# Performance work log

Measured on AMD Instinct MI355X. Metric: run time of the kernel, lower is better.

## Reference

```python
import jax, jax.numpy as jnp
import numpy as np

NUM_SCALES = 4
ENC = 64
KMAX = 16
DT = 0.005  # base_time_constant; original code's (undefined) self.dt interpreted as this


def setup_inputs() -> dict:
    key = jax.random.key(0)
    ks = jax.random.split(key, 5)
    events = jax.random.normal(ks[0], (2, 2, 32, 32, 64), dtype=jnp.float32)
    # matches torch.logspace(-3, -1, num_scales)
    time_constants = jnp.logspace(-3.0, -1.0, NUM_SCALES).astype(jnp.float32)
    temporal_kernels = jax.random.normal(ks[1], (NUM_SCALES, ENC, KMAX), dtype=jnp.float32)
    w1 = jax.random.normal(ks[2], (2 * NUM_SCALES, NUM_SCALES), dtype=jnp.float32) * 0.1
    b1 = jnp.zeros((2 * NUM_SCALES,), dtype=jnp.float32)
    w2 = jax.random.normal(ks[3], (NUM_SCALES, 2 * NUM_SCALES), dtype=jnp.float32) * 0.1
    b2 = jnp.zeros((NUM_SCALES,), dtype=jnp.float32)
    return {"events": events, "time_constants": time_constants,
            "temporal_kernels": temporal_kernels, "w1": w1, "b1": b1, "w2": w2, "b2": b2}


def reference(events, time_constants, temporal_kernels, w1, b1, w2, b2):
    B, C, H, W, T = events.shape
    k = min(KMAX, T)
    # decay kernels per scale: [S, k], normalized to sum 1
    t_idx = jnp.arange(k, dtype=jnp.float32)
    decay = jnp.exp(-t_idx[None, :] * DT / time_constants[:, None])
    decay = decay / decay.sum(axis=-1, keepdims=True)
    # combined learnable kernels: [S, E, k]
    combined = decay[:, None, :] * temporal_kernels[:, :, :k]

    Cf = C * H * W
    # one batched cross-correlation (torch F.conv1d semantics == lax conv, no flip)
    x = events.reshape(B * Cf, 1, T)                       # [B*Cf, 1, T]
    kern = combined.reshape(NUM_SCALES * ENC, 1, k)        # [S*E, 1, k]
    out = jax.lax.conv_general_dilated(
        x, kern, window_strides=(1,), padding=[(k // 2, k // 2)],
        dimension_numbers=("NCH", "OIH", "NCH"))           # [B*Cf, S*E, T+1]
    Tp = out.shape[-1]
    # [B, E, S, Cf, Tp] matching torch stack order (enc at dim1, scale at dim2)
    feats = out.reshape(B, Cf, NUM_SCALES, ENC, Tp).transpose(0, 3, 2, 1, 4)

    # torch .var() is unbiased -> ddof=1
    feature_variance = feats.var(axis=-1, ddof=1).mean(axis=(1, 3))  # [B, S]
    h = jax.nn.relu(feature_variance @ w1.T + b1)
    attn = jax.nn.softmax(h @ w2.T + b2, axis=-1)                    # [B, S]

    encoded = (feats * attn[:, None, :, None, None]).sum(axis=2)     # [B, E, Cf, Tp]
    return encoded
```

## Files before the change

### kernel.cpp

```cpp
#include <hip/hip_runtime.h>

#define CF 2048
#define TT 64
#define TP 65
#define KK 16
#define SS 4
#define EE 64
#define BB 2
#define DT_CONST 0.005f


__global__ void __launch_bounds__(256, 2) kA_gram(const float* __restrict__ events,
                                                  float* __restrict__ ws) {
    __shared__ float xs[16][97];
    __shared__ float S1L[16][16];
    __shared__ float part[16][136];
    const int tid = threadIdx.x;

    {
        const float4* src = reinterpret_cast<const float4*>(
            events + (size_t)blockIdx.x * (16 * TT));
        float4 v = src[tid];
        int r = tid >> 4, c0 = ((tid & 15) << 2) + 8;
        xs[r][c0] = v.x; xs[r][c0+1] = v.y; xs[r][c0+2] = v.z; xs[r][c0+3] = v.w;
        for (int idx = tid; idx < 16 * 33; idx += 256) {
            int rr = idx / 33, k = idx % 33;
            int c = (k < 8) ? k : (k + 64);
            xs[rr][c] = 0.f;
        }
    }
    __syncthreads();

    const int r   = tid >> 4;
    const int lag = tid & 15;

    {
        float s = 0.f;
#pragma unroll
        for (int u = 0; u <= 64; ++u) s += xs[r][lag + u];
        S1L[r][lag] = s;
    }
    __syncthreads();

    {
        const float inv65 = 1.f / 65.f;
        float C = 0.f;
#pragma unroll
        for (int u = 0; u <= 64; ++u) C += xs[r][u] * xs[r][u + lag];
        part[r][lag] = C - S1L[r][0] * S1L[r][lag] * inv65;
#pragma unroll
        for (int d1 = 1; d1 <= 15; ++d1) {
            C += xs[r][64 + d1] * xs[r][64 + d1 + lag]
               - xs[r][d1 - 1]  * xs[r][d1 - 1 + lag];
            if (lag + d1 <= 15) {
                int p = 16 * d1 - ((d1 * (d1 - 1)) >> 1) + lag;
                part[r][p] = C - S1L[r][d1] * S1L[r][d1 + lag] * inv65;
            }
        }
    }
    __syncthreads();

    if (tid < 136) {
        float g = 0.f;
#pragma unroll
        for (int rr = 0; rr < 16; ++rr) g += part[rr][tid];
        ws[blockIdx.x * 136 + tid] = g;
    }
}

__global__ void __launch_bounds__(256, 4) kB2_main(
        const float* __restrict__ events, const float* __restrict__ tc,
        const float* __restrict__ tk, const float* __restrict__ w1,
        const float* __restrict__ b1, const float* __restrict__ w2,
        const float* __restrict__ b2, const float* __restrict__ ws,
        float* __restrict__ out) {
    __shared__ float buf[4672];
    __shared__ float wkL[BB * EE * KK];
    float* Gf    = buf;
    float* combL = buf + 512;
    float* fvL   = buf + 4608;
    const int tid = threadIdx.x;

    for (int V = tid; V < BB * 136; V += 256) {
        int b = V / 136, p = V % 136;
        int pp = p, d1 = 0;
        while (pp >= KK - d1) { pp -= KK - d1; ++d1; }
        int d2 = d1 + pp;
        float acc = 0.f;
#pragma unroll 32
        for (int blk = 0; blk < 128; ++blk)
            acc += ws[(size_t)(b * 128 + blk) * 136 + p];
        Gf[(b * KK + d1) * KK + d2] = acc;
        Gf[(b * KK + d2) * KK + d1] = acc;
    }
    {
        int s = tid >> 6;
        float inv = DT_CONST / tc[s];
        float dk[KK]; float dsum = 0.f;
#pragma unroll
        for (int j = 0; j < KK; ++j) { dk[j] = expf(-(float)j * inv); dsum += dk[j]; }
        float rn = 1.f / dsum;
#pragma unroll
        for (int i = 0; i < 4; ++i) {
            float4 v = reinterpret_cast<const float4*>(tk + tid * KK)[i];
            combL[tid * KK + 4*i + 0] = dk[4*i + 0] * rn * v.x;
            combL[tid * KK + 4*i + 1] = dk[4*i + 1] * rn * v.y;
            combL[tid * KK + 4*i + 2] = dk[4*i + 2] * rn * v.z;
            combL[tid * KK + 4*i + 3] = dk[4*i + 3] * rn * v.w;
        }
    }
    __syncthreads();
    {
        float c[KK];
#pragma unroll
        for (int i = 0; i < 4; ++i) {
            float4 v = reinterpret_cast<const float4*>(combL + tid * KK)[i];
            c[4*i] = v.x; c[4*i+1] = v.y; c[4*i+2] = v.z; c[4*i+3] = v.w;
        }
        float acc0 = 0.f, acc1 = 0.f;
#pragma unroll
        for (int d1 = 0; d1 < KK; ++d1) {
            float cd1 = c[d1];
            float t0 = 0.5f * Gf[d1 * KK + d1] * cd1;
            float t1 = 0.5f * Gf[256 + d1 * KK + d1] * cd1;
#pragma unroll
            for (int d2 = d1 + 1; d2 < KK; ++d2) {
                t0 += Gf[d1 * KK + d2] * c[d2];
                t1 += Gf[256 + d1 * KK + d2] * c[d2];
            }
            acc0 += 2.f * cd1 * t0;
            acc1 += 2.f * cd1 * t1;
        }
#pragma unroll
        for (int sft = 1; sft < 64; sft <<= 1) {
            acc0 += __shfl_xor(acc0, sft, 64);
            acc1 += __shfl_xor(acc1, sft, 64);
        }
        if ((tid & 63) == 0) {
            const float scale = 1.f / 8388608.f;
            fvL[(tid >> 6)]     = acc0 * scale;
            fvL[4 + (tid >> 6)] = acc1 * scale;
        }
    }
    __syncthreads();
    {
        int bt = tid >> 7;
        float fv[SS];
#pragma unroll
        for (int s = 0; s < SS; ++s) fv[s] = fvL[bt * SS + s];
        float h[8];
#pragma unroll
        for (int i = 0; i < 8; ++i) {
            float a = b1[i];
#pragma unroll
            for (int s = 0; s < SS; ++s) a += fv[s] * w1[i * SS + s];
            h[i] = a > 0.f ? a : 0.f;
        }
        float lg[SS]; float mx = -1e30f;
#pragma unroll
        for (int s = 0; s < SS; ++s) {
            float a = b2[s];
#pragma unroll
            for (int i = 0; i < 8; ++i) a += h[i] * w2[s * 8 + i];
            lg[s] = a; mx = fmaxf(mx, a);
        }
        float se = 0.f;
#pragma unroll
        for (int s = 0; s < SS; ++s) { lg[s] = expf(lg[s] - mx); se += lg[s]; }
        float attn[SS];
#pragma unroll
        for (int s = 0; s < SS; ++s) attn[s] = lg[s] / se;
#pragma unroll
        for (int k = 0; k < 8; ++k) {
            int o = tid * 8 + k;
            int e = (o >> 4) & 63, dt2 = o & 15;
            float a = 0.f;
#pragma unroll
            for (int s = 0; s < SS; ++s)
                a += attn[s] * combL[(s * EE + e) * KK + dt2];
            wkL[o] = a;
        }
    }
    __syncthreads();

    const int seg = tid >> 6;
    const int r   = tid & 63;
#pragma unroll 1
    for (int it = 0; it < 4; ++it) {
        const int c2 = blockIdx.x + (it << 10);
        const int be = c2 >> 5;
        const int b  = be >> 6;
        const int rowg = (c2 << 6) + r;
        const float* xr = events + (((size_t)b << 11) + (rowg & (CF - 1))) * TT;

        float wk[KK];
#pragma unroll
        for (int i = 0; i < 4; ++i) {
            float4 v = reinterpret_cast<const float4*>(wkL + be * KK)[i];
            wk[4*i] = v.x; wk[4*i+1] = v.y; wk[4*i+2] = v.z; wk[4*i+3] = v.w;
        }

        float win[32];
        if (seg == 0) {
#pragma unroll
            for (int k = 0; k < 8; ++k) win[k] = 0.f;
#pragma unroll
            for (int k = 0; k < 6; ++k) {
                float4 v = reinterpret_cast<const float4*>(xr)[k];
                win[8+4*k] = v.x; win[9+4*k] = v.y; win[10+4*k] = v.z; win[11+4*k] = v.w;
            }
        } else if (seg == 3) {
#pragma unroll
            for (int k = 0; k < 6; ++k) {
                float4 v = reinterpret_cast<const float4*>(xr + 40)[k];
                win[4*k] = v.x; win[4*k+1] = v.y; win[4*k+2] = v.z; win[4*k+3] = v.w;
            }
#pragma unroll
            for (int k = 24; k < 32; ++k) win[k] = 0.f;
        } else {
            const float* bp2 = xr + (seg == 1 ? 8 : 24);
#pragma unroll
            for (int k = 0; k < 8; ++k) {
                float4 v = reinterpret_cast<const float4*>(bp2)[k];
                win[4*k] = v.x; win[4*k+1] = v.y; win[4*k+2] = v.z; win[4*k+3] = v.w;
            }
        }

        float acc[16];
#pragma unroll
        for (int i = 0; i < 16; ++i) acc[i] = 0.f;
#pragma unroll
        for (int dt = 0; dt < 16; ++dt) {
            float w = wk[dt];
#pragma unroll
            for (int i = 0; i < 16; ++i) acc[i] += w * win[i + dt];
        }
        float acc16 = 0.f;
        if (seg == 3) {
#pragma unroll
            for (int dt = 0; dt < 8; ++dt) acc16 += wk[dt] * win[16 + dt];
        }

        __syncthreads();
        float* bp = buf + r * TP + seg * 16;
#pragma unroll
        for (int i = 0; i < 16; ++i) bp[i] = acc[i];
        if (seg == 3) bp[16] = acc16;
        __syncthreads();

        const float4* bs = reinterpret_cast<const float4*>(buf);
        float4* od = reinterpret_cast<float4*>(out + (size_t)c2 * (64 * TP));
        for (int j = tid; j < 64 * TP / 4; j += 256)
            od[j] = bs[j];
    }
}

extern "C" void kernel_launch(void* const* d_in, const int* in_sizes, int n_in,
                              void* d_out, int out_size, void* d_ws, size_t ws_size,
                              hipStream_t stream) {
    const float* events = (const float*)d_in[0];
    const float* tc     = (const float*)d_in[1];
    const float* tk     = (const float*)d_in[2];
    const float* w1     = (const float*)d_in[3];
    const float* b1     = (const float*)d_in[4];
    const float* w2     = (const float*)d_in[5];
    const float* b2     = (const float*)d_in[6];
    float* out = (float*)d_out;
    float* ws  = (float*)d_ws;

    hipLaunchKernelGGL(kA_gram,  dim3(256),  dim3(256), 0, stream, events, ws);
    hipLaunchKernelGGL(kB2_main, dim3(1024), dim3(256), 0, stream,
                       events, tc, tk, w1, b1, w2, b2, ws, out);
}
```

Baseline: 40.87 us.

## Compute temporal convolution with split-bf16 MFMA and transpose gram workspace layout

Replaces the per-thread FP32 sliding-window convolution with MFMA 16x16x32 bf16 instructions. Both the attention-weighted kernels and the Toeplitz input windows are split into hi/lo bf16 pairs, and three MFMAs recover near-FP32 accuracy. The grid is re-partitioned so each block handles 8 Cf rows of one batch, loading the events into shared memory once. The gram workspace is transposed so the reduction reads contiguous float4 values. The output is written with strided scalar stores instead of contiguous float4 stores, which may hurt write bandwidth; the split-bf16 scheme also risks small accuracy loss.

```diff
diff --git a/kernel.cpp b/kernel.cpp
--- a/kernel.cpp
+++ b/kernel.cpp
@@ -9,6 +9,9 @@
 #define BB 2
 #define DT_CONST 0.005f
 
+typedef float f32x4 __attribute__((ext_vector_type(4)));
+typedef short bf16x8 __attribute__((ext_vector_type(8)));
+
 
 __global__ void __launch_bounds__(256, 2) kA_gram(const float* __restrict__ events,
                                                   float* __restrict__ ws) {
@@ -16,6 +19,7 @@
     __shared__ float S1L[16][16];
     __shared__ float part[16][136];
     const int tid = threadIdx.x;
+    const int bq  = blockIdx.x >> 7;
 
     {
         const float4* src = reinterpret_cast<const float4*>(
@@ -64,34 +68,52 @@
         float g = 0.f;
 #pragma unroll
         for (int rr = 0; rr < 16; ++rr) g += part[rr][tid];
-        ws[blockIdx.x * 136 + tid] = g;
+        ws[((size_t)(bq * 136 + tid)) * 128 + (blockIdx.x & 127)] = g;
     }
 }
 
-__global__ void __launch_bounds__(256, 4) kB2_main(
+__global__ void __launch_bounds__(256, 2) kB3_main(
         const float* __restrict__ events, const float* __restrict__ tc,
         const float* __restrict__ tk, const float* __restrict__ w1,
         const float* __restrict__ b1, const float* __restrict__ w2,
         const float* __restrict__ b2, const float* __restrict__ ws,
         float* __restrict__ out) {
-    __shared__ float buf[4672];
-    __shared__ float wkL[BB * EE * KK];
-    float* Gf    = buf;
-    float* combL = buf + 512;
-    float* fvL   = buf + 4608;
+    __shared__ float U[5248];
+    __shared__ float xs[8 * 97];
+    __shared__ __align__(16) unsigned short wkbh[64 * 32];
+    __shared__ __align__(16) unsigned short wkbl[64 * 32];
+    __shared__ __align__(16) unsigned short BmatTh[80 * 24 + 16];
+    __shared__ __align__(16) unsigned short BmatTl[80 * 24 + 16];
+    float* Gf    = U;
+    float* combL = U + 512;
+    float* fvL   = U + 4608;
     const int tid = threadIdx.x;
-
-    for (int V = tid; V < BB * 136; V += 256) {
-        int b = V / 136, p = V % 136;
+    const int bid = blockIdx.x;
+    const int b   = bid >> 8;
+
+    for (int idx = tid; idx < 8 * 33; idx += 256) {
+        int rr = idx / 33, k = idx % 33;
+        int c = (k < 8) ? k : (k + 64);
+        xs[rr * 97 + c] = 0.f;
+    }
+    if (tid < 128) {
+        float4 v = reinterpret_cast<const float4*>(events + (size_t)bid * 512)[tid];
+        int rr = tid >> 4, c0 = ((tid & 15) << 2) + 8;
+        xs[rr * 97 + c0] = v.x; xs[rr * 97 + c0 + 1] = v.y;
+        xs[rr * 97 + c0 + 2] = v.z; xs[rr * 97 + c0 + 3] = v.w;
+    }
+    for (int v = tid; v < 272; v += 256) {
+        int b2 = (v >= 136) ? 1 : 0;
+        int p  = v - b2 * 136;
         int pp = p, d1 = 0;
         while (pp >= KK - d1) { pp -= KK - d1; ++d1; }
         int d2 = d1 + pp;
+        const float4* rp = reinterpret_cast<const float4*>(ws + (size_t)v * 128);
         float acc = 0.f;
-#pragma unroll 32
-        for (int blk = 0; blk < 128; ++blk)
-            acc += ws[(size_t)(b * 128 + blk) * 136 + p];
-        Gf[(b * KK + d1) * KK + d2] = acc;
-        Gf[(b * KK + d2) * KK + d1] = acc;
+#pragma unroll
+        for (int i = 0; i < 32; ++i) { float4 q = rp[i]; acc += (q.x + q.y) + (q.z + q.w); }
+        Gf[(b2 * KK + d1) * KK + d2] = acc;
+        Gf[(b2 * KK + d2) * KK + d1] = acc;
     }
     {
         int s = tid >> 6;
@@ -110,6 +132,7 @@
         }
     }
     __syncthreads();
+
     {
         float c[KK];
 #pragma unroll
@@ -143,11 +166,11 @@
         }
     }
     __syncthreads();
-    {
-        int bt = tid >> 7;
+
+    {
         float fv[SS];
 #pragma unroll
-        for (int s = 0; s < SS; ++s) fv[s] = fvL[bt * SS + s];
+        for (int s = 0; s < SS; ++s) fv[s] = fvL[b * SS + s];
         float h[8];
 #pragma unroll
         for (int i = 0; i < 8; ++i) {
@@ -171,87 +194,70 @@
 #pragma unroll
         for (int s = 0; s < SS; ++s) attn[s] = lg[s] / se;
 #pragma unroll
-        for (int k = 0; k < 8; ++k) {
-            int o = tid * 8 + k;
-            int e = (o >> 4) & 63, dt2 = o & 15;
+        for (int j = 0; j < 4; ++j) {
+            int idx = tid * 4 + j;
+            int e = idx >> 4, k2 = idx & 15;
             float a = 0.f;
 #pragma unroll
             for (int s = 0; s < SS; ++s)
-                a += attn[s] * combL[(s * EE + e) * KK + dt2];
-            wkL[o] = a;
-        }
-    }
-    __syncthreads();
-
-    const int seg = tid >> 6;
-    const int r   = tid & 63;
+                a += attn[s] * combL[(s * EE + e) * KK + k2];
+            unsigned int bits = __float_as_uint(a);
+            unsigned short hh = (unsigned short)(bits >> 16);
+            float hf = __uint_as_float(((unsigned int)hh) << 16);
+            unsigned short ll = (unsigned short)(__float_as_uint(a - hf) >> 16);
+            wkbh[e * 32 + k2] = hh;      wkbl[e * 32 + k2] = ll;
+            wkbh[e * 32 + 16 + k2] = 0;  wkbl[e * 32 + 16 + k2] = 0;
+        }
+    }
+    __syncthreads();
+
+    const int w   = tid >> 6;
+    const int l   = tid & 63;
+    const int llo = l & 15, lhi = l >> 4;
+    bf16x8 Ah = *reinterpret_cast<const bf16x8*>(&wkbh[(w * 16 + llo) * 32 + 8 * lhi]);
+    bf16x8 Al = *reinterpret_cast<const bf16x8*>(&wkbl[(w * 16 + llo) * 32 + 8 * lhi]);
+    float* stage = U;
+    const size_t obase0 = (size_t)b * 8519680 + (size_t)(bid & 255) * 520;
+
 #pragma unroll 1
-    for (int it = 0; it < 4; ++it) {
-        const int c2 = blockIdx.x + (it << 10);
-        const int be = c2 >> 5;
-        const int b  = be >> 6;
-        const int rowg = (c2 << 6) + r;
-        const float* xr = events + (((size_t)b << 11) + (rowg & (CF - 1))) * TT;
-
-        float wk[KK];
-#pragma unroll
-        for (int i = 0; i < 4; ++i) {
-            float4 v = reinterpret_cast<const float4*>(wkL + be * KK)[i];
-            wk[4*i] = v.x; wk[4*i+1] = v.y; wk[4*i+2] = v.z; wk[4*i+3] = v.w;
-        }
-
-        float win[32];
-        if (seg == 0) {
-#pragma unroll
-            for (int k = 0; k < 8; ++k) win[k] = 0.f;
-#pragma unroll
-            for (int k = 0; k < 6; ++k) {
-                float4 v = reinterpret_cast<const float4*>(xr)[k];
-                win[8+4*k] = v.x; win[9+4*k] = v.y; win[10+4*k] = v.z; win[11+4*k] = v.w;
+    for (int cf = 0; cf < 8; ++cf) {
+        for (int idx = tid; idx < 1280; idx += 256) {
+            int t = idx >> 4, k2 = idx & 15;
+            float x = xs[cf * 97 + t + k2];
+            unsigned int bits = __float_as_uint(x);
+            unsigned short hh = (unsigned short)(bits >> 16);
+            float hf = __uint_as_float(((unsigned int)hh) << 16);
+            unsigned short ll = (unsigned short)(__float_as_uint(x - hf) >> 16);
+            BmatTh[t * 24 + k2] = hh;
+            BmatTl[t * 24 + k2] = ll;
+        }
+        __syncthreads();
+#pragma unroll
+        for (int nt = 0; nt < 5; ++nt) {
+            bf16x8 Bh = *reinterpret_cast<const bf16x8*>(
+                &BmatTh[(nt * 16 + llo) * 24 + 8 * lhi]);
+            bf16x8 Bl = *reinterpret_cast<const bf16x8*>(
+                &BmatTl[(nt * 16 + llo) * 24 + 8 * lhi]);
+            f32x4 acc = {0.f, 0.f, 0.f, 0.f};
+            acc = __builtin_amdgcn_mfma_f32_16x16x32_bf16(Al, Bh, acc, 0, 0, 0);
+            acc = __builtin_amdgcn_mfma_f32_16x16x32_bf16(Ah, Bl, acc, 0, 0, 0);
+            acc = __builtin_amdgcn_mfma_f32_16x16x32_bf16(Ah, Bh, acc, 0, 0, 0);
+#pragma unroll
+            for (int i = 0; i < 4; ++i)
+                stage[(w * 16 + lhi * 4 + i) * 82 + nt * 16 + llo] = acc[i];
+        }
+        __syncthreads();
+        {
+            const size_t ob = obase0 + (size_t)cf * 65;
+            int q = tid >> 6, t = tid & 63;
+#pragma unroll
+            for (int kk = 0; kk < 16; ++kk) {
+                int e = q * 16 + kk;
+                out[ob + (size_t)e * 133120 + t] = stage[e * 82 + t];
             }
-        } else if (seg == 3) {
-#pragma unroll
-            for (int k = 0; k < 6; ++k) {
-                float4 v = reinterpret_cast<const float4*>(xr + 40)[k];
-                win[4*k] = v.x; win[4*k+1] = v.y; win[4*k+2] = v.z; win[4*k+3] = v.w;
-            }
-#pragma unroll
-            for (int k = 24; k < 32; ++k) win[k] = 0.f;
-        } else {
-            const float* bp2 = xr + (seg == 1 ? 8 : 24);
-#pragma unroll
-            for (int k = 0; k < 8; ++k) {
-                float4 v = reinterpret_cast<const float4*>(bp2)[k];
-                win[4*k] = v.x; win[4*k+1] = v.y; win[4*k+2] = v.z; win[4*k+3] = v.w;
-            }
-        }
-
-        float acc[16];
-#pragma unroll
-        for (int i = 0; i < 16; ++i) acc[i] = 0.f;
-#pragma unroll
-        for (int dt = 0; dt < 16; ++dt) {
-            float w = wk[dt];
-#pragma unroll
-            for (int i = 0; i < 16; ++i) acc[i] += w * win[i + dt];
-        }
-        float acc16 = 0.f;
-        if (seg == 3) {
-#pragma unroll
-            for (int dt = 0; dt < 8; ++dt) acc16 += wk[dt] * win[16 + dt];
-        }
-
+            if (tid < 64) out[ob + (size_t)tid * 133120 + 64] = stage[tid * 82 + 64];
+        }
         __syncthreads();
-        float* bp = buf + r * TP + seg * 16;
-#pragma unroll
-        for (int i = 0; i < 16; ++i) bp[i] = acc[i];
-        if (seg == 3) bp[16] = acc16;
-        __syncthreads();
-
-        const float4* bs = reinterpret_cast<const float4*>(buf);
-        float4* od = reinterpret_cast<float4*>(out + (size_t)c2 * (64 * TP));
-        for (int j = tid; j < 64 * TP / 4; j += 256)
-            od[j] = bs[j];
     }
 }
 
@@ -268,7 +274,7 @@
     float* out = (float*)d_out;
     float* ws  = (float*)d_ws;
 
-    hipLaunchKernelGGL(kA_gram,  dim3(256),  dim3(256), 0, stream, events, ws);
-    hipLaunchKernelGGL(kB2_main, dim3(1024), dim3(256), 0, stream,
+    hipLaunchKernelGGL(kA_gram,  dim3(256), dim3(256), 0, stream, events, ws);
+    hipLaunchKernelGGL(kB3_main, dim3(512), dim3(256), 0, stream,
                        events, tc, tk, w1, b1, w2, b2, ws, out);
 }
```

Measured after the change: 36.78 us. 10.0% less time.
